# Optimization experiments

Hardware: AMD Instinct MI355X
Metric: run time of the kernel (lower is better)

## Reference

```python
import jax, jax.numpy as jnp
import numpy as np

T_, B_, C_ = 1, 2, 4
D_, H_, W_ = 32, 32, 32
RES = (16, 16, 16)          # (Dlat, Hlat, Wlat)
K_ = 32                      # fixed max neighbors (pad+mask)
RADIUS = 0.055
OUT_CH = 128
NUM_CH = 32                  # pos-embedding channels per coord
MAXP = 10000.0
EMB = 3 * NUM_CH             # 96


def _pos_embed(coords):
    # transformer sinusoidal embedding: [..., 3] -> [..., 96]
    freq = 1.0 / (MAXP ** (jnp.arange(0, NUM_CH, 2, dtype=jnp.float32) / NUM_CH))  # [16]
    ang = coords[..., None] * freq                                   # [..., 3, 16]
    emb = jnp.concatenate([jnp.sin(ang), jnp.cos(ang)], axis=-1)     # [..., 3, 32]
    return emb.reshape(coords.shape[:-1] + (EMB,))


def _kernel_mlp(h, W0, b0, W1, b1, W2, b2, W3, b3):
    # LinearChannelMLP layers [196,128,256,128,128] with gelu between layers
    h = jax.nn.gelu(h @ W0 + b0)
    h = jax.nn.gelu(h @ W1 + b1)
    h = jax.nn.gelu(h @ W2 + b2)
    return h @ W3 + b3


def _make_input_grid():
    # grid_coords[b] has shape [H, W, D, 3]; flatten matches f_y's (h w d) order
    th = np.linspace(0.0, 1.0, H_, dtype=np.float32)
    tw = np.linspace(0.0, 1.0, W_, dtype=np.float32)
    td = np.linspace(0.0, 1.0, D_, dtype=np.float32)
    Xh, Yw, Zd = np.meshgrid(th, tw, td, indexing='ij')
    return np.stack([Xh, Yw, Zd], axis=-1)  # [H, W, D, 3]


def _make_latent_grid():
    # mirrors __init__: tx over res[1], ty over res[2], tz over res[0]
    tx = np.linspace(0.0, 1.0, RES[1], dtype=np.float32)
    ty = np.linspace(0.0, 1.0, RES[2], dtype=np.float32)
    tz = np.linspace(0.0, 1.0, RES[0], dtype=np.float32)
    X, Y, Z = np.meshgrid(tx, ty, tz, indexing='ij')
    return np.stack([X, Y, Z], axis=-1).reshape(-1, 3)  # [Nq, 3]


def _radius_neighbors(q, y, radius, k):
    # brute-force KDTree replacement: k nearest within radius, padded + masked
    nq = q.shape[0]
    idx = np.zeros((nq, k), np.int32)
    msk = np.zeros((nq, k), bool)
    r2 = radius * radius
    for s in range(0, nq, 512):
        qb = q[s:s + 512]
        d2 = ((qb[:, None, :] - y[None, :, :]) ** 2).sum(-1)  # [chunk, Ny]
        part = np.argpartition(d2, k, axis=1)[:, :k]
        pd = np.take_along_axis(d2, part, 1)
        order = np.argsort(pd, axis=1)
        part = np.take_along_axis(part, order, 1)
        pd = np.take_along_axis(pd, order, 1)
        idx[s:s + 512] = part.astype(np.int32)
        msk[s:s + 512] = pd <= r2
    return idx, msk


def setup_inputs() -> dict:
    key = jax.random.key(0)
    ks = jax.random.split(key, 9)
    x = jax.random.normal(ks[0], (T_, B_, C_, D_, H_, W_), jnp.float32)

    gc = _make_input_grid()                                   # [H,W,D,3]
    grid_coords = jnp.asarray(np.broadcast_to(gc, (B_,) + gc.shape).copy())
    lat = _make_latent_grid()                                 # [Nq,3]
    latent_grid = jnp.asarray(lat)

    # bbox of grid is [0,1]^3 so rescaled latent grid == latent_grid here
    idx, msk = _radius_neighbors(lat, gc.reshape(-1, 3), RADIUS, K_)
    nbr_idx = jnp.asarray(np.broadcast_to(idx, (B_,) + idx.shape).copy())
    nbr_mask = jnp.asarray(np.broadcast_to(msk, (B_,) + msk.shape).copy())

    kin = 2 * EMB + C_  # 196
    def lin(k, fin, fout):
        return jax.random.normal(k, (fin, fout), jnp.float32) / np.float32(np.sqrt(fin))
    W0 = lin(ks[1], kin, 128); b0 = jnp.zeros((128,), jnp.float32)
    W1 = lin(ks[2], 128, 256); b1 = jnp.zeros((256,), jnp.float32)
    W2 = lin(ks[3], 256, 128); b2 = jnp.zeros((128,), jnp.float32)
    W3 = lin(ks[4], 128, OUT_CH); b3 = jnp.zeros((OUT_CH,), jnp.float32)

    return {"x": x, "grid_coords": grid_coords, "latent_grid": latent_grid,
            "nbr_idx": nbr_idx, "nbr_mask": nbr_mask,
            "W0": W0, "b0": b0, "W1": W1, "b1": b1,
            "W2": W2, "b2": b2, "W3": W3, "b3": b3}


def reference(x, grid_coords, latent_grid, nbr_idx, nbr_mask,
              W0, b0, W1, b1, W2, b2, W3, b3):
    T, B, C, D, H, W = x.shape
    Dl, Hl, Wl = RES
    # 't b c d h w -> b t (h w d) c'
    f = jnp.transpose(x, (1, 0, 4, 5, 3, 2)).reshape(B, T, H * W * D, C)
    y = grid_coords.reshape(B, -1, 3)                         # [B,Ny,3]
    bmin = y.min(axis=1, keepdims=True)
    bmax = y.max(axis=1, keepdims=True)
    lat = bmin + (bmax - bmin) * latent_grid[None]            # [B,Nq,3]

    y_emb = _pos_embed(y)                                     # [B,Ny,96]
    x_emb = _pos_embed(lat)                                   # [B,Nq,96]

    def per_batch(y_e, x_e, f_b, idx, msk):
        # gather neighbor features (ragged -> padded fixed-K)
        rep = y_e[idx]                                        # [Nq,K,96]
        slf = jnp.broadcast_to(x_e[:, None, :], rep.shape)    # [Nq,K,96]
        f_nbr = f_b[:, idx]                                   # [T,Nq,K,C]
        coord_feat = jnp.concatenate([rep, slf], axis=-1)     # [Nq,K,192]
        agg = jnp.concatenate(
            [jnp.broadcast_to(coord_feat[None], (f_b.shape[0],) + coord_feat.shape),
             f_nbr], axis=-1)                                 # [T,Nq,K,196]
        k = _kernel_mlp(agg, W0, b0, W1, b1, W2, b2, W3, b3)  # [T,Nq,K,out]
        k = k * msk[None, :, :, None].astype(k.dtype)
        return k.sum(axis=2)                                  # [T,Nq,out] (reduction='sum')

    out = jax.vmap(per_batch)(y_emb, x_emb, f, nbr_idx, nbr_mask)  # [B,T,Nq,out]
    # 'b t (h w d) c -> t b c d h w'
    out = out.reshape(B, T, Hl, Wl, Dl, -1)
    out = jnp.transpose(out, (1, 0, 5, 4, 2, 3))              # [T,B,out,Dl,Hl,Wl]
    return out
```

## Files before the change

### kernel.cpp

```cpp
#include <hip/hip_runtime.h>
#include <hip/hip_bf16.h>
#include <math.h>


typedef short bs8 __attribute__((ext_vector_type(8)));
typedef float f4  __attribute__((ext_vector_type(4)));

#define MFMA16 __builtin_amdgcn_mfma_f32_16x16x32_bf16

#define W0ET_OFF   0u
#define W1T_OFF    24576u
#define W2T_OFF    90112u
#define W3T_OFF    155648u
#define VQ_OFF     188416u
#define GF_OFF     2285568u
#define ST2_OFF    19062784u
#define CNT_OFF    23257088u
#define FAST_NEED  23289856u

#define OW0AT_OFF   0
#define OW1T_OFF    32768
#define OW2T_OFF    98304
#define OW3T_OFF    163840
#define OSTAGED_OFF 196608
#define OLD_NEED    (196608 + 4194304)

__device__ __forceinline__ short f2bf(float f) {
  unsigned u = __float_as_uint(f);
  return (short)((u + 0x7FFFu + ((u >> 16) & 1u)) >> 16);
}
__device__ __forceinline__ float bf2f(short s) {
  return __uint_as_float(((unsigned)(unsigned short)s) << 16);
}
__device__ __forceinline__ unsigned pk2bf(float lo, float hi) {
  __hip_bfloat162 h = __float22bfloat162_rn(float2{lo, hi});
  return *reinterpret_cast<unsigned*>(&h);
}
__device__ __forceinline__ float gelu_t(float x) {
  float t = x * x;
  float z = x * fmaf(0.10294322f, t, 2.3022077f);
  float e = __builtin_exp2f(z);
  float r = __builtin_amdgcn_rcpf(e + 1.0f);
  return fmaf(-r, x, x);
}
__device__ __forceinline__ float gelu_old(float x) {
  float z = 0.7978845608028654f * fmaf(0.044715f * x, x * x, x);
  float e = __expf(2.0f * z);
  return 0.5f * x * (2.0f - 2.0f / (e + 1.0f));
}


__global__ void gno_prep2(const float* __restrict__ W0, const float* __restrict__ W1,
                          const float* __restrict__ W2, const float* __restrict__ W3,
                          short* __restrict__ W0eT, short* __restrict__ W1T,
                          short* __restrict__ W2T, short* __restrict__ W3T) {
  int g = blockIdx.x * 256 + threadIdx.x;
  if (g < 12288) {
    int nn = g / 96, k = g % 96;
    W0eT[g] = f2bf(W0[k * 128 + nn]);
  } else if (g < 45056) {
    int h = g - 12288, nn = h >> 7, k = h & 127;
    W1T[h] = f2bf(W1[k * 256 + nn]);
  } else if (g < 77824) {
    int h = g - 45056, nn = h >> 8, k = h & 255;
    W2T[h] = f2bf(W2[k * 128 + nn]);
  } else if (g < 94208) {
    int h = g - 77824, nn = h >> 7, k = h & 127;
    W3T[h] = f2bf(W3[k * 128 + nn]);
  }
}

__global__ void gno_vq(const float* __restrict__ latg, const float* __restrict__ W0,
                       const float* __restrict__ b0, float* __restrict__ vqPre) {
  __shared__ float embS[2][96];
  __shared__ float latS[2][3];
  __shared__ float freqS[16];
  const int tid = threadIdx.x;
  const int q0 = blockIdx.x * 2;
  if (tid < 16) freqS[tid] = (float)exp(-(double)tid * (9.210340371976184 / 16.0));
  if (tid < 6) latS[tid / 3][tid % 3] = latg[q0 * 3 + tid];
  __syncthreads();
  if (tid < 192) {
    int qh = tid / 96, c = tid % 96, a = c >> 5, jj = c & 31;
    float ca = latS[qh][a];
    embS[qh][c] = (jj < 16) ? __sinf(ca * freqS[jj]) : __cosf(ca * freqS[jj & 15]);
  }
  __syncthreads();
  const int qh = tid >> 7, o = tid & 127;
  float s = b0[o];
#pragma unroll 4
  for (int j = 0; j < 96; ++j) s = fmaf(embS[qh][j], W0[(96 + j) * 128 + o], s);
  vqPre[(q0 + qh) * 128 + o] = s;
}

__global__ __launch_bounds__(256, 4) void gno_gf(
    const float* __restrict__ x, const float* __restrict__ gc, const float* __restrict__ W0,
    const short* __restrict__ W0eT, short* __restrict__ GF) {
  __shared__ __align__(16) short embS[64][104];
  __shared__ float gcS[64][3];
  __shared__ float xS[2][4][64];
  __shared__ float wfS[4][128];
  __shared__ float freqS[16];

  const int tid = threadIdx.x;
  const int n0 = blockIdx.x * 64;
  if (tid < 16) freqS[tid] = (float)exp(-(double)tid * (9.210340371976184 / 16.0));
  if (tid < 192) gcS[tid / 3][tid % 3] = gc[n0 * 3 + tid];
#pragma unroll
  for (int u = 0; u < 2; ++u) {
    int slot = tid * 2 + u;
    int bb = slot >> 8, ch = (slot >> 6) & 3, i = slot & 63;
    int n = n0 + i;
    xS[bb][ch][i] = x[((bb * 4 + ch) << 15) + ((n & 31) << 10) + (n >> 5)];
    wfS[slot >> 7][slot & 127] = W0[(192 + (slot >> 7)) * 128 + (slot & 127)];
  }
  __syncthreads();
  {
    int rr = tid >> 2, c4 = tid & 3;
#pragma unroll
    for (int c = c4 * 24; c < c4 * 24 + 24; ++c) {
      int a = c >> 5, jj = c & 31;
      float v = (jj < 16) ? __sinf(gcS[rr][a] * freqS[jj]) : __cosf(gcS[rr][a] * freqS[jj & 15]);
      embS[rr][c] = f2bf(v);
    }
  }
  __syncthreads();
  const int wid = tid >> 6, lane = tid & 63;
  const int l15 = lane & 15, lg = lane >> 4;
  const int f0 = wid * 32;
  f4 acc[2][4] = {};
#pragma unroll
  for (int ks = 0; ks < 3; ++ks) {
    bs8 Aw[2], Be[4];
#pragma unroll
    for (int ft = 0; ft < 2; ++ft)
      Aw[ft] = *(const bs8*)(W0eT + (f0 + ft * 16 + l15) * 96 + ks * 32 + lg * 8);
#pragma unroll
    for (int pt = 0; pt < 4; ++pt)
      Be[pt] = *(const bs8*)(&embS[pt * 16 + l15][ks * 32 + lg * 8]);
#pragma unroll
    for (int ft = 0; ft < 2; ++ft)
#pragma unroll
      for (int pt = 0; pt < 4; ++pt)
        acc[ft][pt] = MFMA16(Aw[ft], Be[pt], acc[ft][pt], 0, 0, 0);
  }
#pragma unroll
  for (int ft = 0; ft < 2; ++ft) {
    f4 wf0 = *(const f4*)(&wfS[0][f0 + ft * 16 + lg * 4]);
    f4 wf1 = *(const f4*)(&wfS[1][f0 + ft * 16 + lg * 4]);
    f4 wf2 = *(const f4*)(&wfS[2][f0 + ft * 16 + lg * 4]);
    f4 wf3 = *(const f4*)(&wfS[3][f0 + ft * 16 + lg * 4]);
#pragma unroll
    for (int pt = 0; pt < 4; ++pt) {
      int p = pt * 16 + l15;
#pragma unroll
      for (int bb = 0; bb < 2; ++bb) {
        float x0 = xS[bb][0][p], x1 = xS[bb][1][p], x2 = xS[bb][2][p], x3 = xS[bb][3][p];
        float v0 = acc[ft][pt][0] + x0 * wf0[0] + x1 * wf1[0] + x2 * wf2[0] + x3 * wf3[0];
        float v1 = acc[ft][pt][1] + x0 * wf0[1] + x1 * wf1[1] + x2 * wf2[1] + x3 * wf3[1];
        float v2 = acc[ft][pt][2] + x0 * wf0[2] + x1 * wf1[2] + x2 * wf2[2] + x3 * wf3[2];
        float v3 = acc[ft][pt][3] + x0 * wf0[3] + x1 * wf1[3] + x2 * wf2[3] + x3 * wf3[3];
        uint2 pp;
        pp.x = pk2bf(v0, v1);
        pp.y = pk2bf(v2, v3);
        *(uint2*)(GF + ((size_t)((bb << 15) + n0 + p)) * 128 + f0 + ft * 16 + lg * 4) = pp;
      }
    }
  }
}

__device__ __forceinline__ uint4 gelu8(bs8 g, const float* vrow) {
  f4 va = *(const f4*)vrow;
  f4 vb = *(const f4*)(vrow + 4);
  uint4 r;
  r.x = pk2bf(gelu_t(bf2f(g[0]) + va[0]), gelu_t(bf2f(g[1]) + va[1]));
  r.y = pk2bf(gelu_t(bf2f(g[2]) + va[2]), gelu_t(bf2f(g[3]) + va[3]));
  r.z = pk2bf(gelu_t(bf2f(g[4]) + vb[0]), gelu_t(bf2f(g[5]) + vb[1]));
  r.w = pk2bf(gelu_t(bf2f(g[6]) + vb[2]), gelu_t(bf2f(g[7]) + vb[3]));
  return r;
}

__global__ __launch_bounds__(256, 3) void gno_main3(
    const float* __restrict__ gc, const float* __restrict__ latg,
    const int* __restrict__ nidx,
    const float* __restrict__ b1, const float* __restrict__ b2,
    const short* __restrict__ W1T, const short* __restrict__ W2T,
    const float* __restrict__ vqPre, const short* __restrict__ GF,
    float* __restrict__ staged, float* __restrict__ cntG) {
  __shared__ __align__(16) short h0S[64][136];
  __shared__ __align__(16) short h1S[64][264];
  __shared__ float vqS[2][128];
  __shared__ float maskfS[64];

  const int tid = threadIdx.x;
  const int blk = blockIdx.x;
  const int b = blk >> 11;
  const int q0 = (blk & 2047) * 2;

  vqS[tid >> 7][tid & 127] = vqPre[(q0 + (tid >> 7)) * 128 + (tid & 127)];

  const int r = tid >> 2, seg = tid & 3;
  const int qh = r >> 5;
  const int n = nidx[(q0 + qh) * 32 + (r & 31)];
  const bs8* gp = (const bs8*)(GF + ((size_t)((b << 15) + n)) * 128 + seg * 32);
  bs8 g0 = gp[0], g1 = gp[1], g2 = gp[2], g3 = gp[3];
  if (seg == 0) {
    float la = latg[(q0 + qh) * 3], lb = latg[(q0 + qh) * 3 + 1], lc = latg[(q0 + qh) * 3 + 2];
    float d0 = __fsub_rn(la, gc[n * 3]);
    float d1 = __fsub_rn(lb, gc[n * 3 + 1]);
    float d2 = __fsub_rn(lc, gc[n * 3 + 2]);
    float s = __fadd_rn(__fadd_rn(__fmul_rn(d0, d0), __fmul_rn(d1, d1)), __fmul_rn(d2, d2));
    maskfS[r] = ((double)s <= 0.055 * 0.055) ? 1.0f : 0.0f;
  }
  __syncthreads();
  {
    const float* vrow = vqS[qh] + seg * 32;
    *(uint4*)(&h0S[r][seg * 32]) = gelu8(g0, vrow);
    *(uint4*)(&h0S[r][seg * 32 + 8]) = gelu8(g1, vrow + 8);
    *(uint4*)(&h0S[r][seg * 32 + 16]) = gelu8(g2, vrow + 16);
    *(uint4*)(&h0S[r][seg * 32 + 24]) = gelu8(g3, vrow + 24);
  }
  __syncthreads();
  if (tid < 2) {
    float s = 0.0f;
#pragma unroll
    for (int i = 0; i < 32; ++i) s += maskfS[tid * 32 + i];
    cntG[(b << 12) + q0 + tid] = s;
  }

  const int wid = tid >> 6, lane = tid & 63;
  const int l15 = lane & 15, lg = lane >> 4;

  {
    const int f0 = wid * 64;
    f4 acc[4][4] = {};
#pragma unroll
    for (int ks = 0; ks < 4; ++ks) {
      bs8 Bh[4], Aw[4];
#pragma unroll
      for (int rt = 0; rt < 4; ++rt)
        Bh[rt] = *(const bs8*)(&h0S[rt * 16 + l15][ks * 32 + lg * 8]);
#pragma unroll
      for (int ft = 0; ft < 4; ++ft)
        Aw[ft] = *(const bs8*)(W1T + (f0 + ft * 16 + l15) * 128 + ks * 32 + lg * 8);
#pragma unroll
      for (int ft = 0; ft < 4; ++ft)
#pragma unroll
        for (int rt = 0; rt < 4; ++rt)
          acc[ft][rt] = MFMA16(Aw[ft], Bh[rt], acc[ft][rt], 0, 0, 0);
    }
#pragma unroll
    for (int ft = 0; ft < 4; ++ft) {
      f4 bias = *(const f4*)(b1 + f0 + ft * 16 + lg * 4);
#pragma unroll
      for (int rt = 0; rt < 4; ++rt) {
        float v0 = gelu_t(acc[ft][rt][0] + bias[0]);
        float v1 = gelu_t(acc[ft][rt][1] + bias[1]);
        float v2 = gelu_t(acc[ft][rt][2] + bias[2]);
        float v3 = gelu_t(acc[ft][rt][3] + bias[3]);
        uint2 p;
        p.x = pk2bf(v0, v1);
        p.y = pk2bf(v2, v3);
        *(uint2*)(&h1S[rt * 16 + l15][f0 + ft * 16 + lg * 4]) = p;
      }
    }
  }
  __syncthreads();
  {
    const int mh = wid >> 1, nh = wid & 1;
    const int rbase = mh * 32, f0 = nh * 64;
    f4 acc[4][2] = {};
#pragma unroll
    for (int ks = 0; ks < 8; ++ks) {
      bs8 Ah[2], Bw[4];
#pragma unroll
      for (int rt = 0; rt < 2; ++rt)
        Ah[rt] = *(const bs8*)(&h1S[rbase + rt * 16 + l15][ks * 32 + lg * 8]);
#pragma unroll
      for (int ct = 0; ct < 4; ++ct)
        Bw[ct] = *(const bs8*)(W2T + (f0 + ct * 16 + l15) * 256 + ks * 32 + lg * 8);
#pragma unroll
      for (int ct = 0; ct < 4; ++ct)
#pragma unroll
        for (int rt = 0; rt < 2; ++rt)
          acc[ct][rt] = MFMA16(Ah[rt], Bw[ct], acc[ct][rt], 0, 0, 0);
    }
    float psum[4];
#pragma unroll
    for (int ct = 0; ct < 4; ++ct) {
      float bias = b2[f0 + ct * 16 + l15];
      float s = 0.0f;
#pragma unroll
      for (int rt = 0; rt < 2; ++rt)
#pragma unroll
        for (int i = 0; i < 4; ++i) {
          int row = rbase + rt * 16 + lg * 4 + i;
          s += gelu_t(acc[ct][rt][i] + bias) * maskfS[row];
        }
      psum[ct] = s;
    }
#pragma unroll
    for (int ct = 0; ct < 4; ++ct) {
      psum[ct] += __shfl_xor(psum[ct], 16, 64);
      psum[ct] += __shfl_xor(psum[ct], 32, 64);
    }
    if (lane < 16) {
      float* op = staged + ((size_t)((b << 12) + q0 + mh)) * 128 + f0;
      op[lane] = psum[0];
      op[16 + lane] = psum[1];
      op[32 + lane] = psum[2];
      op[48 + lane] = psum[3];
    }
  }
}

__global__ __launch_bounds__(256, 4) void gno_fin(
    const float* __restrict__ staged, const float* __restrict__ cntG,
    const short* __restrict__ W3T, const float* __restrict__ b3,
    float* __restrict__ out) {
  __shared__ float cntS[32];
  const int tid = threadIdx.x, blk = blockIdx.x;
  const int rowbase = blk * 32;
  if (tid < 32) cntS[tid] = cntG[rowbase + tid];
  __syncthreads();
  const int wid = tid >> 6, lane = tid & 63;
  const int l15 = lane & 15, lg = lane >> 4;
  const int f0 = wid * 32;
  f4 acc[2][2] = {};
#pragma unroll
  for (int ks = 0; ks < 4; ++ks) {
    bs8 Aa[2], Bw[2];
#pragma unroll
    for (int rt = 0; rt < 2; ++rt) {
      const float* ap = staged + (size_t)(rowbase + rt * 16 + l15) * 128 + ks * 32 + lg * 8;
      f4 a0 = *(const f4*)ap;
      f4 a1 = *(const f4*)(ap + 4);
      uint4 uu;
      uu.x = pk2bf(a0[0], a0[1]);
      uu.y = pk2bf(a0[2], a0[3]);
      uu.z = pk2bf(a1[0], a1[1]);
      uu.w = pk2bf(a1[2], a1[3]);
      Aa[rt] = *reinterpret_cast<bs8*>(&uu);
    }
#pragma unroll
    for (int ct = 0; ct < 2; ++ct)
      Bw[ct] = *(const bs8*)(W3T + (f0 + ct * 16 + l15) * 128 + ks * 32 + lg * 8);
#pragma unroll
    for (int ct = 0; ct < 2; ++ct)
#pragma unroll
      for (int rt = 0; rt < 2; ++rt)
        acc[ct][rt] = MFMA16(Aa[rt], Bw[ct], acc[ct][rt], 0, 0, 0);
  }
#pragma unroll
  for (int ct = 0; ct < 2; ++ct) {
    int feat = f0 + ct * 16 + l15;
    float bb = b3[feat];
#pragma unroll
    for (int rt = 0; rt < 2; ++rt)
#pragma unroll
      for (int i = 0; i < 4; ++i) {
        int lr = rt * 16 + lg * 4 + i;
        int gq = rowbase + lr;
        int bidx = gq >> 12, q = gq & 4095;
        out[((size_t)bidx << 19) + (feat << 12) + ((q & 15) << 8) + ((q >> 8) << 4) +
            ((q >> 4) & 15)] = acc[ct][rt][i] + cntS[lr] * bb;
      }
  }
}


__global__ void gno_prep(const float* __restrict__ W0, const float* __restrict__ W1,
                         const float* __restrict__ W2, const float* __restrict__ W3,
                         short* __restrict__ W0aT, short* __restrict__ W1T,
                         short* __restrict__ W2T, short* __restrict__ W3T) {
  int g = blockIdx.x * 256 + threadIdx.x;
  if (g < 16384) {
    int n = g >> 7, k = g & 127;
    float v = (k < 96) ? W0[k * 128 + n] : ((k < 100) ? W0[(k + 96) * 128 + n] : 0.0f);
    W0aT[g] = f2bf(v);
  } else if (g < 49152) {
    int h = g - 16384, n = h >> 7, k = h & 127;
    W1T[h] = f2bf(W1[k * 256 + n]);
  } else if (g < 81920) {
    int h = g - 49152, n = h >> 8, k = h & 255;
    W2T[h] = f2bf(W2[k * 128 + n]);
  } else if (g < 98304) {
    int h = g - 81920, n = h >> 7, k = h & 127;
    W3T[h] = f2bf(W3[k * 128 + n]);
  }
}

template <int SIN, int K>
__device__ __forceinline__ void gemm_block(const short* inS, const short* __restrict__ WT,
                                           int colBase, int lane, f4 (&acc)[2][4]) {
  constexpr int KS = K / 32;
  bs8 Bf[2][KS];
  const int bcol = lane & 15;
  const int bk = (lane >> 4) * 8;
#pragma unroll
  for (int ct = 0; ct < 2; ++ct)
#pragma unroll
    for (int ks = 0; ks < KS; ++ks)
      Bf[ct][ks] = *reinterpret_cast<const bs8*>(WT + (colBase + ct * 16 + bcol) * K + ks * 32 + bk);
#pragma unroll
  for (int mt = 0; mt < 4; ++mt) {
#pragma unroll
    for (int ks = 0; ks < KS; ++ks) {
      bs8 Af = *reinterpret_cast<const bs8*>(inS + (mt * 16 + bcol) * SIN + ks * 32 + bk);
      acc[0][mt] = MFMA16(Af, Bf[0][ks], acc[0][mt], 0, 0, 0);
      acc[1][mt] = MFMA16(Af, Bf[1][ks], acc[1][mt], 0, 0, 0);
    }
  }
}

__global__ __launch_bounds__(256, 2) void gno_main(
    const float* __restrict__ x, const float* __restrict__ gc,
    const float* __restrict__ latg, const int* __restrict__ nidx,
    const float* __restrict__ W0, const float* __restrict__ b0,
    const float* __restrict__ b1, const float* __restrict__ b2,
    const float* __restrict__ b3,
    const short* __restrict__ W0aT, const short* __restrict__ W1T,
    const short* __restrict__ W2T, const short* __restrict__ W3T,
    float* __restrict__ dst, int direct) {
  __shared__ __align__(16) short aggS[64][136];
  __shared__ __align__(16) short h0S[64][136];
  __shared__ __align__(16) short h1S[64][264];
  __shared__ float vqS[2][128];
  __shared__ float maskfS[64];
  __shared__ float freqS[16];
  __shared__ float latS[2][3];
  __shared__ float sEmbQ[2][96];

  const int tid = threadIdx.x;
  const int blk = blockIdx.x;
  const int b = blk >> 11;
  const int q0 = (blk & 2047) * 2;

  if (tid < 16) freqS[tid] = (float)exp(-(double)tid * (9.210340371976184 / 16.0));
  if (tid >= 32 && tid < 38) {
    int t = tid - 32, qh = t / 3, a = t % 3;
    latS[qh][a] = latg[(q0 + qh) * 3 + a];
  }
  __syncthreads();
  if (tid < 192) {
    int qh = tid / 96, c = tid % 96, a = c >> 5, jj = c & 31;
    float ca = latS[qh][a];
    sEmbQ[qh][c] = (jj < 16) ? __sinf(ca * freqS[jj]) : __cosf(ca * freqS[jj & 15]);
  }
  __syncthreads();
  {
    int qh = tid >> 7, o = tid & 127;
    float s = b0[o];
#pragma unroll 4
    for (int j = 0; j < 96; ++j) s = fmaf(sEmbQ[qh][j], W0[(96 + j) * 128 + o], s);
    vqS[qh][o] = s;
  }
  {
    int r = tid >> 2, qq = tid & 3;
    int qh = r >> 5, kk = r & 31;
    int n = nidx[(q0 + qh) * 32 + kk];
    float c0 = gc[n * 3], c1 = gc[n * 3 + 1], c2 = gc[n * 3 + 2];
    if (qq == 0) {
      float d0 = __fsub_rn(latS[qh][0], c0);
      float d1 = __fsub_rn(latS[qh][1], c1);
      float d2 = __fsub_rn(latS[qh][2], c2);
      float s = __fadd_rn(__fadd_rn(__fmul_rn(d0, d0), __fmul_rn(d1, d1)), __fmul_rn(d2, d2));
      maskfS[r] = ((double)s <= 0.055 * 0.055) ? 1.0f : 0.0f;
    }
    float cc[3] = {c0, c1, c2};
    for (int c = qq * 34; c < qq * 34 + 34; ++c) {
      float v = 0.0f;
      if (c < 96) {
        int a = c >> 5, jj = c & 31;
        v = (jj < 16) ? __sinf(cc[a] * freqS[jj]) : __cosf(cc[a] * freqS[jj & 15]);
      } else if (c < 100) {
        int ch = c - 96;
        v = x[((b * 4 + ch) << 15) + ((n & 31) << 10) + (n >> 5)];
      }
      aggS[r][c] = f2bf(v);
    }
  }
  __syncthreads();

  const int wave = tid >> 6, lane = tid & 63;
  const int colBase = wave * 32;
  const int lrow4 = (lane >> 4) << 2;
  const int lcol = lane & 15;

  {
    f4 acc[2][4] = {};
    gemm_block<136, 128>(&aggS[0][0], W0aT, colBase, lane, acc);
#pragma unroll
    for (int ct = 0; ct < 2; ++ct) {
      int gcol = colBase + ct * 16 + lcol;
#pragma unroll
      for (int mt = 0; mt < 4; ++mt)
#pragma unroll
        for (int i = 0; i < 4; ++i) {
          int grow = mt * 16 + lrow4 + i;
          h0S[grow][gcol] = f2bf(gelu_old(acc[ct][mt][i] + vqS[grow >> 5][gcol]));
        }
    }
  }
  __syncthreads();
  {
#pragma unroll 1
    for (int cg = 0; cg < 2; ++cg) {
      int cb = wave * 64 + cg * 32;
      f4 acc[2][4] = {};
      gemm_block<136, 128>(&h0S[0][0], W1T, cb, lane, acc);
#pragma unroll
      for (int ct = 0; ct < 2; ++ct) {
        int gcol = cb + ct * 16 + lcol;
        float bias = b1[gcol];
#pragma unroll
        for (int mt = 0; mt < 4; ++mt)
#pragma unroll
          for (int i = 0; i < 4; ++i) {
            int grow = mt * 16 + lrow4 + i;
            h1S[grow][gcol] = f2bf(gelu_old(acc[ct][mt][i] + bias));
          }
      }
    }
  }
  __syncthreads();
  {
    f4 acc[2][4] = {};
    gemm_block<264, 256>(&h1S[0][0], W2T, colBase, lane, acc);
#pragma unroll
    for (int ct = 0; ct < 2; ++ct) {
      int gcol = colBase + ct * 16 + lcol;
      float bias = b2[gcol];
#pragma unroll
      for (int mt = 0; mt < 4; ++mt)
#pragma unroll
        for (int i = 0; i < 4; ++i) {
          int grow = mt * 16 + lrow4 + i;
          aggS[grow][gcol] = f2bf(gelu_old(acc[ct][mt][i] + bias));
        }
    }
  }
  __syncthreads();
  {
    f4 acc[2][4] = {};
    gemm_block<136, 128>(&aggS[0][0], W3T, colBase, lane, acc);
    float part[2][2] = {{0.0f, 0.0f}, {0.0f, 0.0f}};
#pragma unroll
    for (int ct = 0; ct < 2; ++ct) {
      float bias = b3[colBase + ct * 16 + lcol];
#pragma unroll
      for (int mt = 0; mt < 4; ++mt)
#pragma unroll
        for (int i = 0; i < 4; ++i) {
          int grow = mt * 16 + lrow4 + i;
          part[mt >> 1][ct] += (acc[ct][mt][i] + bias) * maskfS[grow];
        }
    }
#pragma unroll
    for (int qh = 0; qh < 2; ++qh)
#pragma unroll
      for (int ct = 0; ct < 2; ++ct) {
        float v = part[qh][ct];
        v += __shfl_xor(v, 16, 64);
        v += __shfl_xor(v, 32, 64);
        if (lane < 16) {
          int o = colBase + ct * 16 + lane;
          int q = q0 + qh;
          if (direct)
            dst[(b << 19) + (o << 12) + ((q & 15) << 8) + ((q >> 8) << 4) + ((q >> 4) & 15)] = v;
          else
            dst[(b * 4096 + q) * 128 + o] = v;
        }
      }
  }
}

__global__ void gno_tr(const float* __restrict__ staged, float* __restrict__ out) {
  __shared__ float tile[16][129];
  int blk = blockIdx.x;
  int b = blk >> 8, i = (blk >> 4) & 15, l = blk & 15;
  int t = threadIdx.x;
  {
    int j = t >> 4, oc = t & 15;
    const float* src = staged + ((b * 4096) + (i * 256 + j * 16 + l)) * 128 + oc * 8;
#pragma unroll
    for (int u = 0; u < 8; ++u) tile[j][oc * 8 + u] = src[u];
  }
  __syncthreads();
  {
    int og = t >> 4, j = t & 15;
#pragma unroll
    for (int oo = 0; oo < 8; ++oo) {
      int o = og * 8 + oo;
      out[(b << 19) + (o << 12) + (l << 8) + (i << 4) + j] = tile[j][o];
    }
  }
}

extern "C" void kernel_launch(void* const* d_in, const int* in_sizes, int n_in,
                              void* d_out, int out_size, void* d_ws, size_t ws_size,
                              hipStream_t stream) {
  const float* x    = (const float*)d_in[0];
  const float* gc   = (const float*)d_in[1];
  const float* latg = (const float*)d_in[2];
  const int*   nidx = (const int*)d_in[3];
  const float* W0 = (const float*)d_in[5];
  const float* b0 = (const float*)d_in[6];
  const float* W1 = (const float*)d_in[7];
  const float* b1 = (const float*)d_in[8];
  const float* W2 = (const float*)d_in[9];
  const float* b2 = (const float*)d_in[10];
  const float* W3 = (const float*)d_in[11];
  const float* b3 = (const float*)d_in[12];

  char* ws = (char*)d_ws;
  float* out = (float*)d_out;

  if (ws_size >= (size_t)FAST_NEED) {
    short* W0eT = (short*)(ws + W0ET_OFF);
    short* W1T  = (short*)(ws + W1T_OFF);
    short* W2T  = (short*)(ws + W2T_OFF);
    short* W3T  = (short*)(ws + W3T_OFF);
    float* vqPre = (float*)(ws + VQ_OFF);
    short* GF   = (short*)(ws + GF_OFF);
    float* staged = (float*)(ws + ST2_OFF);
    float* cntG = (float*)(ws + CNT_OFF);
    gno_prep2<<<368, 256, 0, stream>>>(W0, W1, W2, W3, W0eT, W1T, W2T, W3T);
    gno_vq<<<2048, 256, 0, stream>>>(latg, W0, b0, vqPre);
    gno_gf<<<512, 256, 0, stream>>>(x, gc, W0, W0eT, GF);
    gno_main3<<<4096, 256, 0, stream>>>(gc, latg, nidx, b1, b2,
                                        W1T, W2T, vqPre, GF, staged, cntG);
    gno_fin<<<256, 256, 0, stream>>>(staged, cntG, W3T, b3, out);
  } else {
    short* W0aT = (short*)(ws + OW0AT_OFF);
    short* W1T  = (short*)(ws + OW1T_OFF);
    short* W2T  = (short*)(ws + OW2T_OFF);
    short* W3T  = (short*)(ws + OW3T_OFF);
    float* staged = (float*)(ws + OSTAGED_OFF);
    const bool use_staged = (ws_size >= (size_t)OLD_NEED);
    gno_prep<<<384, 256, 0, stream>>>(W0, W1, W2, W3, W0aT, W1T, W2T, W3T);
    gno_main<<<4096, 256, 0, stream>>>(x, gc, latg, nidx, W0, b0, b1, b2, b3,
                                       W0aT, W1T, W2T, W3T,
                                       use_staged ? staged : out, use_staged ? 0 : 1);
    if (use_staged) gno_tr<<<512, 256, 0, stream>>>(staged, out);
  }
}
```

Before: 235.8 us.

## Merge prep kernels, chunk layer-1/2 to halve LDS, and coalesce output stores

Merges the three preprocessing kernels (weight conversion, per-query embedding projection, per-point feature projection) into one launch with block ranges. W0 is converted into LDS locally, and GF writes are staged through shared memory so they go out as full rows. The main kernel computes layer 1 in two 128-feature chunks and accumulates layer 2 across them, which halves the h1 LDS buffer so occupancy can go from 3 to 4 blocks. The final kernel uses larger tiles and transposes through LDS for coalesced float4 output writes. The trade-offs are more barriers, the W1 tile being recomputed per chunk, and only 32 blocks in the final kernel.

```diff
diff --git a/kernel.cpp b/kernel.cpp
--- a/kernel.cpp
+++ b/kernel.cpp
@@ -8,15 +8,14 @@
 
 #define MFMA16 __builtin_amdgcn_mfma_f32_16x16x32_bf16
 
-#define W0ET_OFF   0u
-#define W1T_OFF    24576u
-#define W2T_OFF    90112u
-#define W3T_OFF    155648u
-#define VQ_OFF     188416u
-#define GF_OFF     2285568u
-#define ST2_OFF    19062784u
-#define CNT_OFF    23257088u
-#define FAST_NEED  23289856u
+#define W1T_OFF    0u
+#define W2T_OFF    65536u
+#define W3T_OFF    131072u
+#define VQ_OFF     163840u
+#define GF_OFF     2260992u
+#define ST_OFF     19038208u
+#define CNT_OFF    23232512u
+#define FAST_NEED  23265280u
 
 #define OW0AT_OFF   0
 #define OW1T_OFF    32768
@@ -50,69 +49,77 @@
 }
 
 
-__global__ void gno_prep2(const float* __restrict__ W0, const float* __restrict__ W1,
-                          const float* __restrict__ W2, const float* __restrict__ W3,
-                          short* __restrict__ W0eT, short* __restrict__ W1T,
-                          short* __restrict__ W2T, short* __restrict__ W3T) {
-  int g = blockIdx.x * 256 + threadIdx.x;
-  if (g < 12288) {
-    int nn = g / 96, k = g % 96;
-    W0eT[g] = f2bf(W0[k * 128 + nn]);
-  } else if (g < 45056) {
-    int h = g - 12288, nn = h >> 7, k = h & 127;
-    W1T[h] = f2bf(W1[k * 256 + nn]);
-  } else if (g < 77824) {
-    int h = g - 45056, nn = h >> 8, k = h & 255;
-    W2T[h] = f2bf(W2[k * 128 + nn]);
-  } else if (g < 94208) {
-    int h = g - 77824, nn = h >> 7, k = h & 127;
-    W3T[h] = f2bf(W3[k * 128 + nn]);
-  }
-}
-
-__global__ void gno_vq(const float* __restrict__ latg, const float* __restrict__ W0,
-                       const float* __restrict__ b0, float* __restrict__ vqPre) {
-  __shared__ float embS[2][96];
-  __shared__ float latS[2][3];
-  __shared__ float freqS[16];
+__global__ __launch_bounds__(256, 2) void gno_pre(
+    const float* __restrict__ x, const float* __restrict__ gc,
+    const float* __restrict__ latg,
+    const float* __restrict__ W0, const float* __restrict__ b0,
+    const float* __restrict__ W1, const float* __restrict__ W2,
+    const float* __restrict__ W3,
+    short* __restrict__ W1T, short* __restrict__ W2T, short* __restrict__ W3T,
+    float* __restrict__ vqPre, short* __restrict__ GF) {
+  __shared__ __align__(16) char smem[45056];
   const int tid = threadIdx.x;
-  const int q0 = blockIdx.x * 2;
+  const int blk = blockIdx.x;
+
+  if (blk < 320) {
+    int g = blk * 256 + tid;
+    if (g < 32768) {
+      int nn = g >> 7, k = g & 127;
+      W1T[g] = f2bf(W1[k * 256 + nn]);
+    } else if (g < 65536) {
+      int h = g - 32768, nn = h >> 8, k = h & 255;
+      W2T[h] = f2bf(W2[k * 128 + nn]);
+    } else {
+      int h = g - 65536, nn = h >> 7, k = h & 127;
+      W3T[h] = f2bf(W3[k * 128 + nn]);
+    }
+    return;
+  }
+
+  if (blk < 2368) {
+    float* embQ  = (float*)smem;
+    float* latS  = (float*)(smem + 768);
+    float* freqS = (float*)(smem + 800);
+    const int q0 = (blk - 320) * 2;
+    if (tid < 16) freqS[tid] = (float)exp(-(double)tid * (9.210340371976184 / 16.0));
+    if (tid < 6) latS[tid] = latg[q0 * 3 + tid];
+    __syncthreads();
+    if (tid < 192) {
+      int qh = tid / 96, c = tid % 96, a = c >> 5, jj = c & 31;
+      float ca = latS[qh * 3 + a];
+      embQ[qh * 96 + c] = (jj < 16) ? __sinf(ca * freqS[jj]) : __cosf(ca * freqS[jj & 15]);
+    }
+    __syncthreads();
+    const int qh = tid >> 7, o = tid & 127;
+    float s = b0[o];
+#pragma unroll 4
+    for (int j = 0; j < 96; ++j) s = fmaf(embQ[qh * 96 + j], W0[(96 + j) * 128 + o], s);
+    vqPre[(q0 + qh) * 128 + o] = s;
+    return;
+  }
+
+  short* w0eS  = (short*)smem;
+  short* embS  = (short*)(smem + 26624);
+  float* gcS   = (float*)(smem + 39936);
+  float* xS    = (float*)(smem + 40704);
+  float* wfS   = (float*)(smem + 42752);
+  float* freqS = (float*)(smem + 44800);
+  short* tileS = w0eS;
+
+  const int n0 = (blk - 2368) * 64;
   if (tid < 16) freqS[tid] = (float)exp(-(double)tid * (9.210340371976184 / 16.0));
-  if (tid < 6) latS[tid / 3][tid % 3] = latg[q0 * 3 + tid];
-  __syncthreads();
-  if (tid < 192) {
-    int qh = tid / 96, c = tid % 96, a = c >> 5, jj = c & 31;
-    float ca = latS[qh][a];
-    embS[qh][c] = (jj < 16) ? __sinf(ca * freqS[jj]) : __cosf(ca * freqS[jj & 15]);
-  }
-  __syncthreads();
-  const int qh = tid >> 7, o = tid & 127;
-  float s = b0[o];
-#pragma unroll 4
-  for (int j = 0; j < 96; ++j) s = fmaf(embS[qh][j], W0[(96 + j) * 128 + o], s);
-  vqPre[(q0 + qh) * 128 + o] = s;
-}
-
-__global__ __launch_bounds__(256, 4) void gno_gf(
-    const float* __restrict__ x, const float* __restrict__ gc, const float* __restrict__ W0,
-    const short* __restrict__ W0eT, short* __restrict__ GF) {
-  __shared__ __align__(16) short embS[64][104];
-  __shared__ float gcS[64][3];
-  __shared__ float xS[2][4][64];
-  __shared__ float wfS[4][128];
-  __shared__ float freqS[16];
-
-  const int tid = threadIdx.x;
-  const int n0 = blockIdx.x * 64;
-  if (tid < 16) freqS[tid] = (float)exp(-(double)tid * (9.210340371976184 / 16.0));
-  if (tid < 192) gcS[tid / 3][tid % 3] = gc[n0 * 3 + tid];
+  if (tid < 192) gcS[tid] = gc[n0 * 3 + tid];
 #pragma unroll
   for (int u = 0; u < 2; ++u) {
     int slot = tid * 2 + u;
     int bb = slot >> 8, ch = (slot >> 6) & 3, i = slot & 63;
     int n = n0 + i;
-    xS[bb][ch][i] = x[((bb * 4 + ch) << 15) + ((n & 31) << 10) + (n >> 5)];
-    wfS[slot >> 7][slot & 127] = W0[(192 + (slot >> 7)) * 128 + (slot & 127)];
+    xS[(bb * 4 + ch) * 64 + i] = x[((bb * 4 + ch) << 15) + ((n & 31) << 10) + (n >> 5)];
+    wfS[(slot >> 7) * 128 + (slot & 127)] = W0[(192 + (slot >> 7)) * 128 + (slot & 127)];
+  }
+  for (int e = tid; e < 12288; e += 256) {
+    int k = e >> 7, f = e & 127;
+    w0eS[f * 104 + k] = f2bf(W0[e]);
   }
   __syncthreads();
   {
@@ -120,8 +127,9 @@
 #pragma unroll
     for (int c = c4 * 24; c < c4 * 24 + 24; ++c) {
       int a = c >> 5, jj = c & 31;
-      float v = (jj < 16) ? __sinf(gcS[rr][a] * freqS[jj]) : __cosf(gcS[rr][a] * freqS[jj & 15]);
-      embS[rr][c] = f2bf(v);
+      float v = (jj < 16) ? __sinf(gcS[rr * 3 + a] * freqS[jj])
+                          : __cosf(gcS[rr * 3 + a] * freqS[jj & 15]);
+      embS[rr * 104 + c] = f2bf(v);
     }
   }
   __syncthreads();
@@ -134,28 +142,30 @@
     bs8 Aw[2], Be[4];
 #pragma unroll
     for (int ft = 0; ft < 2; ++ft)
-      Aw[ft] = *(const bs8*)(W0eT + (f0 + ft * 16 + l15) * 96 + ks * 32 + lg * 8);
+      Aw[ft] = *(const bs8*)(w0eS + (f0 + ft * 16 + l15) * 104 + ks * 32 + lg * 8);
 #pragma unroll
     for (int pt = 0; pt < 4; ++pt)
-      Be[pt] = *(const bs8*)(&embS[pt * 16 + l15][ks * 32 + lg * 8]);
+      Be[pt] = *(const bs8*)(embS + (pt * 16 + l15) * 104 + ks * 32 + lg * 8);
 #pragma unroll
     for (int ft = 0; ft < 2; ++ft)
 #pragma unroll
       for (int pt = 0; pt < 4; ++pt)
         acc[ft][pt] = MFMA16(Aw[ft], Be[pt], acc[ft][pt], 0, 0, 0);
   }
-#pragma unroll
-  for (int ft = 0; ft < 2; ++ft) {
-    f4 wf0 = *(const f4*)(&wfS[0][f0 + ft * 16 + lg * 4]);
-    f4 wf1 = *(const f4*)(&wfS[1][f0 + ft * 16 + lg * 4]);
-    f4 wf2 = *(const f4*)(&wfS[2][f0 + ft * 16 + lg * 4]);
-    f4 wf3 = *(const f4*)(&wfS[3][f0 + ft * 16 + lg * 4]);
-#pragma unroll
-    for (int pt = 0; pt < 4; ++pt) {
-      int p = pt * 16 + l15;
-#pragma unroll
-      for (int bb = 0; bb < 2; ++bb) {
-        float x0 = xS[bb][0][p], x1 = xS[bb][1][p], x2 = xS[bb][2][p], x3 = xS[bb][3][p];
+  __syncthreads();
+#pragma unroll 1
+  for (int bb = 0; bb < 2; ++bb) {
+#pragma unroll
+    for (int ft = 0; ft < 2; ++ft) {
+      f4 wf0 = *(const f4*)(wfS + 0 * 128 + f0 + ft * 16 + lg * 4);
+      f4 wf1 = *(const f4*)(wfS + 1 * 128 + f0 + ft * 16 + lg * 4);
+      f4 wf2 = *(const f4*)(wfS + 2 * 128 + f0 + ft * 16 + lg * 4);
+      f4 wf3 = *(const f4*)(wfS + 3 * 128 + f0 + ft * 16 + lg * 4);
+#pragma unroll
+      for (int pt = 0; pt < 4; ++pt) {
+        int p = pt * 16 + l15;
+        float x0 = xS[(bb * 4 + 0) * 64 + p], x1 = xS[(bb * 4 + 1) * 64 + p];
+        float x2 = xS[(bb * 4 + 2) * 64 + p], x3 = xS[(bb * 4 + 3) * 64 + p];
         float v0 = acc[ft][pt][0] + x0 * wf0[0] + x1 * wf1[0] + x2 * wf2[0] + x3 * wf3[0];
         float v1 = acc[ft][pt][1] + x0 * wf0[1] + x1 * wf1[1] + x2 * wf2[1] + x3 * wf3[1];
         float v2 = acc[ft][pt][2] + x0 * wf0[2] + x1 * wf1[2] + x2 * wf2[2] + x3 * wf3[2];
@@ -163,9 +173,20 @@
         uint2 pp;
         pp.x = pk2bf(v0, v1);
         pp.y = pk2bf(v2, v3);
-        *(uint2*)(GF + ((size_t)((bb << 15) + n0 + p)) * 128 + f0 + ft * 16 + lg * 4) = pp;
-      }
-    }
+        *(uint2*)(tileS + p * 132 + f0 + ft * 16 + lg * 4) = pp;
+      }
+    }
+    __syncthreads();
+    {
+      int row = tid >> 2, c4 = tid & 3;
+      const short* src = tileS + row * 132 + c4 * 32;
+      short* dst = GF + ((size_t)((bb << 15) + n0 + row)) * 128 + c4 * 32;
+      *(uint4*)(dst)      = *(const uint4*)(src);
+      *(uint4*)(dst + 8)  = *(const uint4*)(src + 8);
+      *(uint4*)(dst + 16) = *(const uint4*)(src + 16);
+      *(uint4*)(dst + 24) = *(const uint4*)(src + 24);
+    }
+    __syncthreads();
   }
 }
 
@@ -180,7 +201,7 @@
   return r;
 }
 
-__global__ __launch_bounds__(256, 3) void gno_main3(
+__global__ __launch_bounds__(256, 4) void gno_main4(
     const float* __restrict__ gc, const float* __restrict__ latg,
     const int* __restrict__ nidx,
     const float* __restrict__ b1, const float* __restrict__ b2,
@@ -188,7 +209,7 @@
     const float* __restrict__ vqPre, const short* __restrict__ GF,
     float* __restrict__ staged, float* __restrict__ cntG) {
   __shared__ __align__(16) short h0S[64][136];
-  __shared__ __align__(16) short h1S[64][264];
+  __shared__ __align__(16) short h1S[64][136];
   __shared__ float vqS[2][128];
   __shared__ float maskfS[64];
 
@@ -230,72 +251,81 @@
 
   const int wid = tid >> 6, lane = tid & 63;
   const int l15 = lane & 15, lg = lane >> 4;
-
-  {
-    const int f0 = wid * 64;
-    f4 acc[4][4] = {};
-#pragma unroll
-    for (int ks = 0; ks < 4; ++ks) {
-      bs8 Bh[4], Aw[4];
-#pragma unroll
-      for (int rt = 0; rt < 4; ++rt)
-        Bh[rt] = *(const bs8*)(&h0S[rt * 16 + l15][ks * 32 + lg * 8]);
-#pragma unroll
-      for (int ft = 0; ft < 4; ++ft)
-        Aw[ft] = *(const bs8*)(W1T + (f0 + ft * 16 + l15) * 128 + ks * 32 + lg * 8);
-#pragma unroll
-      for (int ft = 0; ft < 4; ++ft)
+  const int mh = wid >> 1, nh = wid & 1;
+  f4 accL2[4][2] = {};
+
+#pragma unroll 1
+  for (int c = 0; c < 2; ++c) {
+    {
+      const int f0l = wid * 32;
+      const int fg = c * 128 + f0l;
+      f4 acc[2][4] = {};
+#pragma unroll
+      for (int ks = 0; ks < 4; ++ks) {
+        bs8 Aw[2], Bh[4];
+#pragma unroll
+        for (int ft = 0; ft < 2; ++ft)
+          Aw[ft] = *(const bs8*)(W1T + (fg + ft * 16 + l15) * 128 + ks * 32 + lg * 8);
 #pragma unroll
         for (int rt = 0; rt < 4; ++rt)
-          acc[ft][rt] = MFMA16(Aw[ft], Bh[rt], acc[ft][rt], 0, 0, 0);
-    }
-#pragma unroll
-    for (int ft = 0; ft < 4; ++ft) {
-      f4 bias = *(const f4*)(b1 + f0 + ft * 16 + lg * 4);
-#pragma unroll
-      for (int rt = 0; rt < 4; ++rt) {
-        float v0 = gelu_t(acc[ft][rt][0] + bias[0]);
-        float v1 = gelu_t(acc[ft][rt][1] + bias[1]);
-        float v2 = gelu_t(acc[ft][rt][2] + bias[2]);
-        float v3 = gelu_t(acc[ft][rt][3] + bias[3]);
-        uint2 p;
-        p.x = pk2bf(v0, v1);
-        p.y = pk2bf(v2, v3);
-        *(uint2*)(&h1S[rt * 16 + l15][f0 + ft * 16 + lg * 4]) = p;
-      }
-    }
-  }
-  __syncthreads();
-  {
-    const int mh = wid >> 1, nh = wid & 1;
-    const int rbase = mh * 32, f0 = nh * 64;
-    f4 acc[4][2] = {};
-#pragma unroll
-    for (int ks = 0; ks < 8; ++ks) {
-      bs8 Ah[2], Bw[4];
+          Bh[rt] = *(const bs8*)(&h0S[rt * 16 + l15][ks * 32 + lg * 8]);
+#pragma unroll
+        for (int ft = 0; ft < 2; ++ft)
+#pragma unroll
+          for (int rt = 0; rt < 4; ++rt)
+            acc[ft][rt] = MFMA16(Aw[ft], Bh[rt], acc[ft][rt], 0, 0, 0);
+      }
+#pragma unroll
+      for (int ft = 0; ft < 2; ++ft) {
+        f4 bias = *(const f4*)(b1 + fg + ft * 16 + lg * 4);
+#pragma unroll
+        for (int rt = 0; rt < 4; ++rt) {
+          float v0 = gelu_t(acc[ft][rt][0] + bias[0]);
+          float v1 = gelu_t(acc[ft][rt][1] + bias[1]);
+          float v2 = gelu_t(acc[ft][rt][2] + bias[2]);
+          float v3 = gelu_t(acc[ft][rt][3] + bias[3]);
+          uint2 p;
+          p.x = pk2bf(v0, v1);
+          p.y = pk2bf(v2, v3);
+          *(uint2*)(&h1S[rt * 16 + l15][f0l + ft * 16 + lg * 4]) = p;
+        }
+      }
+    }
+    __syncthreads();
+    {
+      const int fo = nh * 64;
+#pragma unroll
+      for (int ks = 0; ks < 4; ++ks) {
+        bs8 Ah[2], Bw[4];
+#pragma unroll
+        for (int rt = 0; rt < 2; ++rt)
+          Ah[rt] = *(const bs8*)(&h1S[mh * 32 + rt * 16 + l15][ks * 32 + lg * 8]);
+#pragma unroll
+        for (int ct = 0; ct < 4; ++ct)
+          Bw[ct] = *(const bs8*)(W2T + (fo + ct * 16 + l15) * 256 + c * 128 + ks * 32 + lg * 8);
+#pragma unroll
+        for (int ct = 0; ct < 4; ++ct)
+#pragma unroll
+          for (int rt = 0; rt < 2; ++rt)
+            accL2[ct][rt] = MFMA16(Ah[rt], Bw[ct], accL2[ct][rt], 0, 0, 0);
+      }
+    }
+    __syncthreads();
+  }
+
+  {
+    const int fo = nh * 64;
+    float psum[4];
+#pragma unroll
+    for (int ct = 0; ct < 4; ++ct) {
+      float bias = b2[fo + ct * 16 + l15];
+      float s = 0.0f;
 #pragma unroll
       for (int rt = 0; rt < 2; ++rt)
-        Ah[rt] = *(const bs8*)(&h1S[rbase + rt * 16 + l15][ks * 32 + lg * 8]);
-#pragma unroll
-      for (int ct = 0; ct < 4; ++ct)
-        Bw[ct] = *(const bs8*)(W2T + (f0 + ct * 16 + l15) * 256 + ks * 32 + lg * 8);
-#pragma unroll
-      for (int ct = 0; ct < 4; ++ct)
-#pragma unroll
-        for (int rt = 0; rt < 2; ++rt)
-          acc[ct][rt] = MFMA16(Ah[rt], Bw[ct], acc[ct][rt], 0, 0, 0);
-    }
-    float psum[4];
-#pragma unroll
-    for (int ct = 0; ct < 4; ++ct) {
-      float bias = b2[f0 + ct * 16 + l15];
-      float s = 0.0f;
-#pragma unroll
-      for (int rt = 0; rt < 2; ++rt)
 #pragma unroll
         for (int i = 0; i < 4; ++i) {
-          int row = rbase + rt * 16 + lg * 4 + i;
-          s += gelu_t(acc[ct][rt][i] + bias) * maskfS[row];
+          int row = mh * 32 + rt * 16 + lg * 4 + i;
+          s += gelu_t(accL2[ct][rt][i] + bias) * maskfS[row];
         }
       psum[ct] = s;
     }
@@ -305,7 +335,7 @@
       psum[ct] += __shfl_xor(psum[ct], 32, 64);
     }
     if (lane < 16) {
-      float* op = staged + ((size_t)((b << 12) + q0 + mh)) * 128 + f0;
+      float* op = staged + ((size_t)((b << 12) + q0 + mh)) * 128 + fo;
       op[lane] = psum[0];
       op[16 + lane] = psum[1];
       op[32 + lane] = psum[2];
@@ -314,25 +344,31 @@
   }
 }
 
-__global__ __launch_bounds__(256, 4) void gno_fin(
+__global__ __launch_bounds__(256, 2) void gno_fin2(
     const float* __restrict__ staged, const float* __restrict__ cntG,
     const short* __restrict__ W3T, const float* __restrict__ b3,
     float* __restrict__ out) {
-  __shared__ float cntS[32];
+  __shared__ __align__(16) float tileS[16 * 260];
+  __shared__ float cntS[256];
+  __shared__ float b3S[128];
   const int tid = threadIdx.x, blk = blockIdx.x;
-  const int rowbase = blk * 32;
-  if (tid < 32) cntS[tid] = cntG[rowbase + tid];
+  const int b = blk >> 4;
+  const int q0 = (blk & 15) * 256;
+  const int hi = blk & 15;
+  cntS[tid] = cntG[(b << 12) + q0 + tid];
+  if (tid < 128) b3S[tid] = b3[tid];
   __syncthreads();
   const int wid = tid >> 6, lane = tid & 63;
   const int l15 = lane & 15, lg = lane >> 4;
-  const int f0 = wid * 32;
-  f4 acc[2][2] = {};
+  const int r0 = wid * 64;
+  f4 acc[8][4] = {};
 #pragma unroll
   for (int ks = 0; ks < 4; ++ks) {
-    bs8 Aa[2], Bw[2];
-#pragma unroll
-    for (int rt = 0; rt < 2; ++rt) {
-      const float* ap = staged + (size_t)(rowbase + rt * 16 + l15) * 128 + ks * 32 + lg * 8;
+    bs8 Aa[4];
+#pragma unroll
+    for (int rt = 0; rt < 4; ++rt) {
+      const float* ap =
+          staged + ((size_t)(b << 12) + q0 + r0 + rt * 16 + l15) * 128 + ks * 32 + lg * 8;
       f4 a0 = *(const f4*)ap;
       f4 a1 = *(const f4*)(ap + 4);
       uint4 uu;
@@ -343,28 +379,41 @@
       Aa[rt] = *reinterpret_cast<bs8*>(&uu);
     }
 #pragma unroll
-    for (int ct = 0; ct < 2; ++ct)
-      Bw[ct] = *(const bs8*)(W3T + (f0 + ct * 16 + l15) * 128 + ks * 32 + lg * 8);
-#pragma unroll
-    for (int ct = 0; ct < 2; ++ct)
-#pragma unroll
-      for (int rt = 0; rt < 2; ++rt)
-        acc[ct][rt] = MFMA16(Aa[rt], Bw[ct], acc[ct][rt], 0, 0, 0);
-  }
-#pragma unroll
-  for (int ct = 0; ct < 2; ++ct) {
-    int feat = f0 + ct * 16 + l15;
-    float bb = b3[feat];
-#pragma unroll
-    for (int rt = 0; rt < 2; ++rt)
+    for (int ct = 0; ct < 8; ++ct) {
+      bs8 Bw = *(const bs8*)(W3T + (ct * 16 + l15) * 128 + ks * 32 + lg * 8);
+#pragma unroll
+      for (int rt = 0; rt < 4; ++rt)
+        acc[ct][rt] = MFMA16(Bw, Aa[rt], acc[ct][rt], 0, 0, 0);
+    }
+  }
+#pragma unroll 1
+  for (int ct = 0; ct < 8; ++ct) {
+#pragma unroll
+    for (int rt = 0; rt < 4; ++rt) {
+      int rr = r0 + rt * 16 + l15;
+      float cv = cntS[rr];
 #pragma unroll
       for (int i = 0; i < 4; ++i) {
-        int lr = rt * 16 + lg * 4 + i;
-        int gq = rowbase + lr;
-        int bidx = gq >> 12, q = gq & 4095;
-        out[((size_t)bidx << 19) + (feat << 12) + ((q & 15) << 8) + ((q >> 8) << 4) +
-            ((q >> 4) & 15)] = acc[ct][rt][i] + cntS[lr] * bb;
-      }
+        int fl = lg * 4 + i;
+        tileS[fl * 260 + rr] = acc[ct][rt][i] + cv * b3S[ct * 16 + fl];
+      }
+    }
+    __syncthreads();
+    {
+      int fl = tid >> 4, dl = tid & 15;
+      int o = ct * 16 + fl;
+      float* dst = out + ((size_t)b << 19) + (o << 12) + (dl << 8) + (hi << 4);
+#pragma unroll
+      for (int w4 = 0; w4 < 4; ++w4) {
+        float4 t;
+        t.x = tileS[fl * 260 + (w4 * 4 + 0) * 16 + dl];
+        t.y = tileS[fl * 260 + (w4 * 4 + 1) * 16 + dl];
+        t.z = tileS[fl * 260 + (w4 * 4 + 2) * 16 + dl];
+        t.w = tileS[fl * 260 + (w4 * 4 + 3) * 16 + dl];
+        *(float4*)(dst + w4 * 4) = t;
+      }
+    }
+    __syncthreads();
   }
 }
 
@@ -617,20 +666,18 @@
   float* out = (float*)d_out;
 
   if (ws_size >= (size_t)FAST_NEED) {
-    short* W0eT = (short*)(ws + W0ET_OFF);
-    short* W1T  = (short*)(ws + W1T_OFF);
-    short* W2T  = (short*)(ws + W2T_OFF);
-    short* W3T  = (short*)(ws + W3T_OFF);
+    short* W1T = (short*)(ws + W1T_OFF);
+    short* W2T = (short*)(ws + W2T_OFF);
+    short* W3T = (short*)(ws + W3T_OFF);
     float* vqPre = (float*)(ws + VQ_OFF);
-    short* GF   = (short*)(ws + GF_OFF);
-    float* staged = (float*)(ws + ST2_OFF);
+    short* GF = (short*)(ws + GF_OFF);
+    float* staged = (float*)(ws + ST_OFF);
     float* cntG = (float*)(ws + CNT_OFF);
-    gno_prep2<<<368, 256, 0, stream>>>(W0, W1, W2, W3, W0eT, W1T, W2T, W3T);
-    gno_vq<<<2048, 256, 0, stream>>>(latg, W0, b0, vqPre);
-    gno_gf<<<512, 256, 0, stream>>>(x, gc, W0, W0eT, GF);
-    gno_main3<<<4096, 256, 0, stream>>>(gc, latg, nidx, b1, b2,
+    gno_pre<<<2880, 256, 0, stream>>>(x, gc, latg, W0, b0, W1, W2, W3,
+                                      W1T, W2T, W3T, vqPre, GF);
+    gno_main4<<<4096, 256, 0, stream>>>(gc, latg, nidx, b1, b2,
                                         W1T, W2T, vqPre, GF, staged, cntG);
-    gno_fin<<<256, 256, 0, stream>>>(staged, cntG, W3T, b3, out);
+    gno_fin2<<<32, 256, 0, stream>>>(staged, cntG, W3T, b3, out);
   } else {
     short* W0aT = (short*)(ws + OW0AT_OFF);
     short* W1T  = (short*)(ws + OW1T_OFF);
```

Measured after the change: 284.5 us. +20.6%, slower.
